# Performance work log

Hardware: AMD Instinct MI355X
Metric: run time of the kernel (lower is better)

Reference implementation:

```python
import jax, jax.numpy as jnp
import numpy as np

K = 20
EPS = 1e-5  # BatchNorm eps
SLOPE = 0.2  # LeakyReLU negative slope


def _lrelu(y):
    return jnp.where(y > 0, y, SLOPE * y)


def _knn_idx(x):
    # x: [B, C, N] -> idx [B, N, K] of nearest neighbors (largest of negative sq dist)
    inner = -2.0 * jnp.einsum('bcn,bcm->bnm', x, x)
    xx = jnp.sum(x * x, axis=1)  # [B, N]
    pd = -xx[:, :, None] - inner - xx[:, None, :]  # [B, N, N]
    return jax.lax.top_k(pd, K)[1]


def _graph_feature(x):
    # x: [B, C, N] -> [B, 2C, N, K] = cat(neighbor - center, center)
    idx = _knn_idx(x)
    xt = jnp.transpose(x, (0, 2, 1))  # [B, N, C]
    nb = jax.vmap(lambda f, i: f[i])(xt, idx)  # [B, N, K, C]
    ctr = xt[:, :, None, :]
    feat = jnp.concatenate([nb - ctr, jnp.broadcast_to(ctr, nb.shape)], axis=-1)
    return jnp.transpose(feat, (0, 3, 1, 2))


def _bn(y, p, ch_axis):
    g, b, m, v = p[0], p[1], p[2], p[3]
    shape = [1] * y.ndim
    shape[ch_axis] = -1
    scale = (g / jnp.sqrt(v + EPS)).reshape(shape)
    return (y - m.reshape(shape)) * scale + b.reshape(shape)


def _conv_block(x, w, bn):
    f = _graph_feature(x)  # [B, 2C_in, N, K]
    y = jnp.einsum('bcnk,oc->bonk', f, w)  # 1x1 conv, no bias
    y = _lrelu(_bn(y, bn, 1))
    return jnp.max(y, axis=-1)  # max over K neighbors -> [B, C_out, N]


def setup_inputs() -> dict:
    key = jax.random.key(0)
    ks = jax.random.split(key, 20)
    B, N = 8, 1024
    inp = {
        'x': jax.random.normal(ks[0], (B, 3, N), jnp.float32),
        'w0': jax.random.normal(ks[1], (64, 6), jnp.float32) * 0.1,
        'w1': jax.random.normal(ks[2], (64, 128), jnp.float32) * 0.1,
        'w2': jax.random.normal(ks[3], (128, 128), jnp.float32) * 0.1,
        'w3': jax.random.normal(ks[4], (256, 256), jnp.float32) * 0.1,
        'bn0': jax.random.uniform(ks[5], (4, 64), jnp.float32) + 0.1,
        'bn1': jax.random.uniform(ks[6], (4, 64), jnp.float32) + 0.1,
        'bn2': jax.random.uniform(ks[7], (4, 128), jnp.float32) + 0.1,
        'bn3': jax.random.uniform(ks[8], (4, 256), jnp.float32) + 0.1,
        'we': jax.random.normal(ks[9], (1024, 512), jnp.float32) * 0.05,
        'bne': jax.random.uniform(ks[10], (4, 1024), jnp.float32) + 0.1,
        'wf0': jax.random.normal(ks[11], (512, 2048), jnp.float32) * 0.02,
        'bnf0': jax.random.uniform(ks[12], (4, 512), jnp.float32) + 0.1,
        'wf1': jax.random.normal(ks[13], (256, 512), jnp.float32) * 0.05,
        'bnf1': jax.random.uniform(ks[14], (4, 256), jnp.float32) + 0.1,
        'wfin': jax.random.normal(ks[15], (64, 256), jnp.float32) * 0.05,
        'bfin': jax.random.normal(ks[16], (64,), jnp.float32) * 0.05,
    }
    return inp


def reference(x, w0, w1, w2, w3, bn0, bn1, bn2, bn3, we, bne, wf0, bnf0, wf1, bnf1, wfin, bfin):
    B = x.shape[0]
    x1 = _conv_block(x, w0, bn0)   # [B, 64, N]
    x2 = _conv_block(x1, w1, bn1)  # [B, 64, N]
    x3 = _conv_block(x2, w2, bn2)  # [B, 128, N]
    x4 = _conv_block(x3, w3, bn3)  # [B, 256, N]
    cat = jnp.concatenate([x1, x2, x3, x4], axis=1)  # [B, 512, N]
    e = _lrelu(_bn(jnp.einsum('bcn,oc->bon', cat, we), bne, 1))  # [B, 1024, N]
    p1 = jnp.max(e, axis=-1)
    p2 = jnp.mean(e, axis=-1)
    h = jnp.concatenate([p1, p2], axis=1)  # [B, 2048]
    h = _lrelu(_bn(h @ wf0.T, bnf0, 1))  # [B, 512]; dropout is eval-mode identity
    h = _lrelu(_bn(h @ wf1.T, bnf1, 1))  # [B, 256]
    return h @ wfin.T + bfin  # [B, 64]
```

## Files before the change

kernel.cpp:

```cpp
#include <hip/hip_runtime.h>
#include <math.h>

#define N_PTS 1024
#define BATCH 8
#define KNN 20
#define EPSB 1e-5f
#define SLOPE 0.2f

typedef __attribute__((ext_vector_type(8))) short short8;
typedef __attribute__((ext_vector_type(4))) float f32x4;
typedef unsigned short ushort_t;
typedef unsigned long long u64;

__device__ __forceinline__ float lrelu(float y) { return y > 0.f ? y : SLOPE * y; }

__device__ __forceinline__ ushort_t f2bf(float f) {
    union { float f; unsigned u; } v; v.f = f;
    unsigned r = v.u + 0x7FFF + ((v.u >> 16) & 1);
    return (ushort_t)(r >> 16);
}

__device__ __forceinline__ void wprep_one(const float* __restrict__ w, float* __restrict__ wpt,
                                          int C, int Cout, int g) {
    int M2 = 2 * Cout;
    if (g >= C * M2) return;
    int c = g / M2, m = g - c * M2;
    float v;
    if (m < Cout) v = w[(size_t)m * 2 * C + c];
    else { int o = m - Cout; v = w[(size_t)o * 2 * C + C + c] - w[(size_t)o * 2 * C + c]; }
    wpt[(size_t)c * M2 + m] = v;
}

__global__ void prep_kernel(const float* __restrict__ we, ushort_t* __restrict__ weh,
                            const float* __restrict__ w0, float* __restrict__ wpt0,
                            const float* __restrict__ w1, float* __restrict__ wpt1,
                            const float* __restrict__ w2, float* __restrict__ wpt2,
                            const float* __restrict__ w3, float* __restrict__ wpt3) {
    int bx = blockIdx.x, tid = threadIdx.x;
    if (bx < 512) {
        int g = bx * 256 + tid;
        float4 v = ((const float4*)we)[g];
        ushort4 o;
        o.x = f2bf(v.x); o.y = f2bf(v.y); o.z = f2bf(v.z); o.w = f2bf(v.w);
        ((ushort4*)weh)[g] = o;
    } else if (bx < 514) {
        wprep_one(w0, wpt0, 3, 64, (bx - 512) * 256 + tid);
    } else if (bx < 546) {
        wprep_one(w1, wpt1, 64, 64, (bx - 514) * 256 + tid);
    } else if (bx < 610) {
        wprep_one(w2, wpt2, 64, 128, (bx - 546) * 256 + tid);
    } else {
        wprep_one(w3, wpt3, 128, 256, (bx - 610) * 256 + tid);
    }
}

__global__ void __launch_bounds__(64)
xx_kernel(const float* __restrict__ x, float* __restrict__ xx, int C, int bstride) {
    int b = blockIdx.y;
    int n = blockIdx.x * 64 + threadIdx.x;
    const float* xb = x + (size_t)b * bstride + n;
    float s = 0.f;
    #pragma unroll 4
    for (int c = 0; c < C; c++) { float v = xb[(size_t)c * N_PTS]; s += v * v; }
    xx[b * N_PTS + n] = s;
}

__global__ void __launch_bounds__(256)
pdabv_kernel(const float* __restrict__ x, const float* __restrict__ wpt,
             const float* __restrict__ xx,
             float* __restrict__ pd, float* __restrict__ A, float* __restrict__ Bv,
             int C, int Cout, int bstride, int pdTiles) {
    int b = blockIdx.z;
    int nt = blockIdx.y;
    int bx = blockIdx.x;
    int tid = threadIdx.x;
    int tx = tid & 15, ty = tid >> 4;
    int n0 = nt * 128;
    __shared__ float sU1[16][128];
    const float* xb = x + (size_t)b * bstride;
    float acc[8][8] = {};

    bool isPd = bx < pdTiles;
    int m0 = isPd ? bx * 128 : (bx - pdTiles) * 128;
    const float* Abase = isPd ? (xb + n0) : (wpt + m0);
    int Astride = isPd ? N_PTS : 2 * Cout;
    const float* Bbase = isPd ? (xb + m0) : (xb + n0);

    int fr = tid >> 5, fcol = (tid & 31) * 4;
    for (int c0 = 0; c0 < C; c0 += 16) {
        int kmax = C - c0; if (kmax > 16) kmax = 16;
        {
            float4 z = {0.f, 0.f, 0.f, 0.f};
            int ca = c0 + fr, cb2 = c0 + fr + 8;
            float4 v0 = (ca < C) ? *(const float4*)&Bbase[(size_t)ca * N_PTS + fcol] : z;
            float4 v1 = (cb2 < C) ? *(const float4*)&Bbase[(size_t)cb2 * N_PTS + fcol] : z;
            *(float4*)&sU1[fr][fcol] = v0;
            *(float4*)&sU1[fr + 8][fcol] = v1;
        }
        __syncthreads();
        if (kmax == 16) {
            #pragma unroll 4
            for (int k = 0; k < 16; k++) {
                const float* ap = Abase + (size_t)(c0 + k) * Astride;
                float4 a0 = *(const float4*)&ap[ty * 4];
                float4 a1 = *(const float4*)&ap[64 + ty * 4];
                float4 b0 = *(const float4*)&sU1[k][tx * 4];
                float4 b1 = *(const float4*)&sU1[k][64 + tx * 4];
                float av[8] = {a0.x, a0.y, a0.z, a0.w, a1.x, a1.y, a1.z, a1.w};
                float bw[8] = {b0.x, b0.y, b0.z, b0.w, b1.x, b1.y, b1.z, b1.w};
                #pragma unroll
                for (int i = 0; i < 8; i++)
                    #pragma unroll
                    for (int j = 0; j < 8; j++) acc[i][j] += av[i] * bw[j];
            }
        } else {
            for (int k = 0; k < kmax; k++) {
                const float* ap = Abase + (size_t)(c0 + k) * Astride;
                float4 a0 = *(const float4*)&ap[ty * 4];
                float4 a1 = *(const float4*)&ap[64 + ty * 4];
                float4 b0 = *(const float4*)&sU1[k][tx * 4];
                float4 b1 = *(const float4*)&sU1[k][64 + tx * 4];
                float av[8] = {a0.x, a0.y, a0.z, a0.w, a1.x, a1.y, a1.z, a1.w};
                float bw[8] = {b0.x, b0.y, b0.z, b0.w, b1.x, b1.y, b1.z, b1.w};
                #pragma unroll
                for (int i = 0; i < 8; i++)
                    #pragma unroll
                    for (int j = 0; j < 8; j++) acc[i][j] += av[i] * bw[j];
            }
        }
        __syncthreads();
    }

    if (isPd) {
        float xm[8];
        const float* xxb = xx + b * N_PTS + m0;
        *(float4*)&xm[0] = *(const float4*)&xxb[tx * 4];
        *(float4*)&xm[4] = *(const float4*)&xxb[64 + tx * 4];
        #pragma unroll
        for (int i = 0; i < 8; i++) {
            int n = n0 + (i >> 2) * 64 + ty * 4 + (i & 3);
            float* prow = pd + ((size_t)(b * N_PTS + n)) * N_PTS;
            for (int jh = 0; jh < 2; jh++) {
                float4 o;
                o.x = 2.f * acc[i][jh * 4 + 0] - xm[jh * 4 + 0];
                o.y = 2.f * acc[i][jh * 4 + 1] - xm[jh * 4 + 1];
                o.z = 2.f * acc[i][jh * 4 + 2] - xm[jh * 4 + 2];
                o.w = 2.f * acc[i][jh * 4 + 3] - xm[jh * 4 + 3];
                *(float4*)&prow[m0 + jh * 64 + tx * 4] = o;
            }
        }
    } else {
        #pragma unroll
        for (int i = 0; i < 8; i++) {
            int rowm = m0 + (i >> 2) * 64 + ty * 4 + (i & 3);
            float* dst = (rowm < Cout) ? (A + ((size_t)b * Cout + rowm) * N_PTS)
                                       : (Bv + ((size_t)b * Cout + rowm - Cout) * N_PTS);
            for (int jh = 0; jh < 2; jh++) {
                float4 o;
                o.x = acc[i][jh * 4 + 0];
                o.y = acc[i][jh * 4 + 1];
                o.z = acc[i][jh * 4 + 2];
                o.w = acc[i][jh * 4 + 3];
                *(float4*)&dst[n0 + jh * 64 + tx * 4] = o;
            }
        }
    }
}

__global__ void __launch_bounds__(256)
topk_kernel(const float* __restrict__ pd, int* __restrict__ idx) {
    int wid = threadIdx.x >> 6;
    int row = blockIdx.x * 4 + wid;
    int lane = threadIdx.x & 63;
    __shared__ u64 Sk[4][64];
    const float* p = pd + (size_t)row * N_PTS;
    float v[16];
    for (int q = 0; q < 4; q++) {
        float4 t = *(const float4*)&p[lane * 16 + q * 4];
        v[q * 4 + 0] = t.x; v[q * 4 + 1] = t.y; v[q * 4 + 2] = t.z; v[q * 4 + 3] = t.w;
    }
    float lmax = v[0];
    #pragma unroll
    for (int j = 1; j < 16; j++) lmax = fmaxf(lmax, v[j]);
    float s = lmax;
    #pragma unroll
    for (int k = 2; k <= 64; k <<= 1) {
        #pragma unroll
        for (int j = k >> 1; j > 0; j >>= 1) {
            float o = __shfl_xor(s, j, 64);
            bool takeMin = (((lane & k) == 0) == ((lane & j) == 0));
            float mn = fminf(s, o), mx = fmaxf(s, o);
            s = takeMin ? mn : mx;
        }
    }
    float tp = __shfl(s, 44, 64);
    unsigned hm = 0;
    #pragma unroll
    for (int j = 0; j < 16; j++) hm |= (v[j] >= tp ? 1u : 0u) << j;
    int cnt = __popc(hm);
    int incl = cnt;
    #pragma unroll
    for (int d = 1; d < 64; d <<= 1) {
        int o = __shfl_up(incl, d, 64);
        if (lane >= d) incl += o;
    }
    int total = __shfl(incl, 63, 64);
    int pos = incl - cnt;
    if (total <= 64) {
        #pragma unroll
        for (int j = 0; j < 16; j++) {
            if (hm & (1u << j)) {
                unsigned u = __float_as_uint(v[j]);
                unsigned msk = ((unsigned)((int)u >> 31)) | 0x80000000u;
                Sk[wid][pos] = ((u64)(u ^ msk) << 32) | (unsigned)(1023 - (lane * 16 + j));
                pos++;
            }
        }
        u64 key = (lane < total) ? Sk[wid][lane] : 0ull;
        #pragma unroll
        for (int k = 2; k <= 64; k <<= 1) {
            #pragma unroll
            for (int j = k >> 1; j > 0; j >>= 1) {
                u64 o = __shfl_xor(key, j, 64);
                bool takeMin = (((lane & k) == 0) == ((lane & j) == 0));
                bool sgt = key > o;
                key = (sgt != takeMin) ? key : o;
            }
        }
        if (lane >= 44) {
            int m = 1023 - (int)(unsigned)(key & 0xFFFFFFFFu);
            idx[row * KNN + (63 - lane)] = m;
        }
    } else {
        for (int kk = 0; kk < KNN; kk++) {
            float bv = v[0]; int bj = 0;
            #pragma unroll
            for (int j = 1; j < 16; j++) if (v[j] > bv) { bv = v[j]; bj = j; }
            int bi = lane * 16 + bj;
            for (int d = 32; d > 0; d >>= 1) {
                float ov = __shfl_down(bv, d, 64);
                int oi = __shfl_down(bi, d, 64);
                if (ov > bv || (ov == bv && oi < bi)) { bv = ov; bi = oi; }
            }
            bi = __shfl(bi, 0, 64);
            if ((bi >> 4) == lane) {
                #pragma unroll
                for (int j = 0; j < 16; j++) if (j == (bi & 15)) v[j] = -INFINITY;
            }
            if (lane == 0) idx[row * KNN + kk] = bi;
        }
    }
}

__global__ void __launch_bounds__(256)
topk0_kernel(const float* __restrict__ x, int* __restrict__ idx) {
    int wid = threadIdx.x >> 6;
    int row = blockIdx.x * 4 + wid;
    int lane = threadIdx.x & 63;
    __shared__ u64 Sk[4][64];
    int b = row >> 10, n = row & 1023;
    const float* xb = x + (size_t)b * 3 * N_PTS;
    float xr0 = xb[n], xr1 = xb[N_PTS + n], xr2 = xb[2 * N_PTS + n];
    float v[16];
    for (int q = 0; q < 4; q++) {
        int base = lane * 16 + q * 4;
        float4 c0 = *(const float4*)&xb[base];
        float4 c1 = *(const float4*)&xb[N_PTS + base];
        float4 c2 = *(const float4*)&xb[2 * N_PTS + base];
        float a0[4] = {c0.x, c0.y, c0.z, c0.w};
        float a1[4] = {c1.x, c1.y, c1.z, c1.w};
        float a2[4] = {c2.x, c2.y, c2.z, c2.w};
        #pragma unroll
        for (int j = 0; j < 4; j++) {
            float d = 0.f;
            d += xr0 * a0[j]; d += xr1 * a1[j]; d += xr2 * a2[j];
            float sq = 0.f;
            sq += a0[j] * a0[j]; sq += a1[j] * a1[j]; sq += a2[j] * a2[j];
            v[q * 4 + j] = 2.f * d - sq;
        }
    }
    float lmax = v[0];
    #pragma unroll
    for (int j = 1; j < 16; j++) lmax = fmaxf(lmax, v[j]);
    float s = lmax;
    #pragma unroll
    for (int k = 2; k <= 64; k <<= 1) {
        #pragma unroll
        for (int j = k >> 1; j > 0; j >>= 1) {
            float o = __shfl_xor(s, j, 64);
            bool takeMin = (((lane & k) == 0) == ((lane & j) == 0));
            float mn = fminf(s, o), mx = fmaxf(s, o);
            s = takeMin ? mn : mx;
        }
    }
    float tp = __shfl(s, 44, 64);
    unsigned hm = 0;
    #pragma unroll
    for (int j = 0; j < 16; j++) hm |= (v[j] >= tp ? 1u : 0u) << j;
    int cnt = __popc(hm);
    int incl = cnt;
    #pragma unroll
    for (int d = 1; d < 64; d <<= 1) {
        int o = __shfl_up(incl, d, 64);
        if (lane >= d) incl += o;
    }
    int total = __shfl(incl, 63, 64);
    int pos = incl - cnt;
    if (total <= 64) {
        #pragma unroll
        for (int j = 0; j < 16; j++) {
            if (hm & (1u << j)) {
                unsigned u = __float_as_uint(v[j]);
                unsigned msk = ((unsigned)((int)u >> 31)) | 0x80000000u;
                Sk[wid][pos] = ((u64)(u ^ msk) << 32) | (unsigned)(1023 - (lane * 16 + j));
                pos++;
            }
        }
        u64 key = (lane < total) ? Sk[wid][lane] : 0ull;
        #pragma unroll
        for (int k = 2; k <= 64; k <<= 1) {
            #pragma unroll
            for (int j = k >> 1; j > 0; j >>= 1) {
                u64 o = __shfl_xor(key, j, 64);
                bool takeMin = (((lane & k) == 0) == ((lane & j) == 0));
                bool sgt = key > o;
                key = (sgt != takeMin) ? key : o;
            }
        }
        if (lane >= 44) {
            int m = 1023 - (int)(unsigned)(key & 0xFFFFFFFFu);
            idx[row * KNN + (63 - lane)] = m;
        }
    } else {
        for (int kk = 0; kk < KNN; kk++) {
            float bv = v[0]; int bj = 0;
            #pragma unroll
            for (int j = 1; j < 16; j++) if (v[j] > bv) { bv = v[j]; bj = j; }
            int bi = lane * 16 + bj;
            for (int d = 32; d > 0; d >>= 1) {
                float ov = __shfl_down(bv, d, 64);
                int oi = __shfl_down(bi, d, 64);
                if (ov > bv || (ov == bv && oi < bi)) { bv = ov; bi = oi; }
            }
            bi = __shfl(bi, 0, 64);
            if ((bi >> 4) == lane) {
                #pragma unroll
                for (int j = 0; j < 16; j++) if (j == (bi & 15)) v[j] = -INFINITY;
            }
            if (lane == 0) idx[row * KNN + kk] = bi;
        }
    }
}

__global__ void __launch_bounds__(256)
gmax_kernel(const float* __restrict__ A, const float* __restrict__ Bv,
            const int* __restrict__ idx, const float* __restrict__ bnp,
            float* __restrict__ out, int Cout, int outStrideB) {
    int b = blockIdx.z;
    int n0 = blockIdx.x * 64;
    int o0 = blockIdx.y * 4;
    int tid = threadIdx.x;
    __shared__ int sidx[64 * 21];
    __shared__ float sA[4][N_PTS];
    for (int t = tid; t < 64 * KNN; t += 256) {
        int nl = t / KNN, k = t - nl * KNN;
        sidx[nl * 21 + k] = idx[(b * N_PTS + n0) * KNN + t];
    }
    const float* Abase = A + ((size_t)b * Cout + o0) * N_PTS;
    for (int q = 0; q < 4; q++) {
        int f = q * 256 + tid;
        int r = f >> 8, c4 = (f & 255) * 4;
        *(float4*)&sA[r][c4] = *(const float4*)&Abase[(size_t)r * N_PTS + c4];
    }
    __syncthreads();
    int nl = tid & 63, ol = tid >> 6;
    float best = -INFINITY;
    #pragma unroll
    for (int k = 0; k < KNN; k++) {
        int j = sidx[nl * 21 + k];
        best = fmaxf(best, sA[ol][j]);
    }
    int o = o0 + ol;
    int n = n0 + nl;
    float pre = best + Bv[((size_t)b * Cout + o) * N_PTS + n];
    float g = bnp[o], bb = bnp[Cout + o], m = bnp[2 * Cout + o], vv = bnp[3 * Cout + o];
    float scale = g / sqrtf(vv + EPSB);
    out[(size_t)b * outStrideB + (size_t)o * N_PTS + n] = lrelu((pre - m) * scale + bb);
}

__global__ void catT_kernel(const float* __restrict__ cat, ushort_t* __restrict__ catT) {
    int b = blockIdx.z, ct = blockIdx.y, nt = blockIdx.x;
    int tid = threadIdx.x;
    __shared__ float tile[64][65];
    const float* cb = cat + (size_t)b * 512 * N_PTS;
    for (int q = 0; q < 16; q++) {
        int e = q * 256 + tid;
        int c = e >> 6, n = e & 63;
        tile[c][n] = cb[(size_t)(ct * 64 + c) * N_PTS + nt * 64 + n];
    }
    __syncthreads();
    for (int q = 0; q < 16; q++) {
        int e = q * 256 + tid;
        int n = e >> 6, c = e & 63;
        catT[((size_t)b * N_PTS + nt * 64 + n) * 512 + ct * 64 + c] = f2bf(tile[c][n]);
    }
}

__global__ void __launch_bounds__(256)
gemm6_mfma(const ushort_t* __restrict__ weh, const ushort_t* __restrict__ catT,
           const float* __restrict__ bne,
           float* __restrict__ pmax, float* __restrict__ psum) {
    int b = blockIdx.z, ot = blockIdx.y, nt = blockIdx.x;
    int tid = threadIdx.x;
    int w = tid >> 6, lane = tid & 63, q = lane >> 4, lr = lane & 15;
    int mblk = w >> 1, nblk = w & 1;
    __shared__ __align__(16) ushort_t sA[128 * 40];
    __shared__ __align__(16) ushort_t sB[128 * 40];
    __shared__ float sa[128], sc[128];
    __shared__ float redmax[128][2], redsum[128][2];
    int o0 = ot * 128, n0 = nt * 128;
    if (tid < 128) {
        int o = o0 + tid;
        float g = bne[o], bb = bne[1024 + o], m = bne[2048 + o], vv = bne[3072 + o];
        float scale = g / sqrtf(vv + EPSB);
        sa[tid] = scale; sc[tid] = bb - m * scale;
    }
    f32x4 acc[4][4] = {};
    const ushort_t* cT = catT + (size_t)b * N_PTS * 512;
    int r0 = tid >> 2, s = tid & 3;
    for (int k0 = 0; k0 < 512; k0 += 32) {
        __syncthreads();
        for (int h = 0; h < 2; h++) {
            int r = r0 + h * 64;
            *(short8*)&sA[r * 40 + s * 8] = *(const short8*)(weh + (size_t)(o0 + r) * 512 + k0 + s * 8);
            *(short8*)&sB[r * 40 + s * 8] = *(const short8*)(cT  + (size_t)(n0 + r) * 512 + k0 + s * 8);
        }
        __syncthreads();
        short8 af[4], bfr[4];
        for (int mi = 0; mi < 4; mi++)
            af[mi] = *(const short8*)&sA[(mblk * 64 + mi * 16 + lr) * 40 + q * 8];
        for (int ni = 0; ni < 4; ni++)
            bfr[ni] = *(const short8*)&sB[(nblk * 64 + ni * 16 + lr) * 40 + q * 8];
        for (int mi = 0; mi < 4; mi++)
            for (int ni = 0; ni < 4; ni++)
                acc[mi][ni] = __builtin_amdgcn_mfma_f32_16x16x32_bf16(af[mi], bfr[ni], acc[mi][ni], 0, 0, 0);
    }
    for (int mi = 0; mi < 4; mi++) {
        for (int r = 0; r < 4; r++) {
            int row = mblk * 64 + mi * 16 + q * 4 + r;
            float a = sa[row], c = sc[row];
            float mx = -INFINITY, sm = 0.f;
            for (int ni = 0; ni < 4; ni++) {
                float y = lrelu(acc[mi][ni][r] * a + c);
                mx = fmaxf(mx, y); sm += y;
            }
            for (int msk = 1; msk < 16; msk <<= 1) {
                mx = fmaxf(mx, __shfl_xor(mx, msk, 16));
                sm += __shfl_xor(sm, msk, 16);
            }
            if (lr == 0) { redmax[row][nblk] = mx; redsum[row][nblk] = sm; }
        }
    }
    __syncthreads();
    if (tid < 128) {
        float mx = fmaxf(redmax[tid][0], redmax[tid][1]);
        float sm = redsum[tid][0] + redsum[tid][1];
        int o = o0 + tid;
        pmax[((size_t)(b * 1024 + o)) * 8 + nt] = mx;
        psum[((size_t)(b * 1024 + o)) * 8 + nt] = sm;
    }
}

__global__ void pool_reduce_kernel(const float* __restrict__ pmax, const float* __restrict__ psum,
                                   float* __restrict__ h0) {
    int g = blockIdx.x * 256 + threadIdx.x;
    int b = g >> 10, o = g & 1023;
    float mx = -INFINITY, sm = 0.f;
    for (int t = 0; t < 8; t++) { mx = fmaxf(mx, pmax[g * 8 + t]); sm += psum[g * 8 + t]; }
    h0[(size_t)b * 2048 + o] = mx;
    h0[(size_t)b * 2048 + 1024 + o] = sm * (1.0f / 1024.0f);
}

__global__ void fc_kernel(const float* __restrict__ in, const float* __restrict__ w,
                          const float* __restrict__ bnp, const float* __restrict__ bias,
                          float* __restrict__ out, int Cin, int Cout, int mode) {
    int blk = blockIdx.x;
    int b = blk / Cout, o = blk % Cout;
    int lane = threadIdx.x;
    const float* inb = in + (size_t)b * Cin;
    const float* wo = w + (size_t)o * Cin;
    float acc = 0.f;
    for (int c = lane; c < Cin; c += 64) acc += inb[c] * wo[c];
    for (int s = 32; s > 0; s >>= 1) acc += __shfl_down(acc, s, 64);
    if (lane == 0) {
        float y = acc;
        if (mode == 0) {
            float g = bnp[o], bb = bnp[Cout + o], m = bnp[2 * Cout + o], vv = bnp[3 * Cout + o];
            y = lrelu((y - m) * (g / sqrtf(vv + EPSB)) + bb);
        } else {
            y += bias[o];
        }
        out[(size_t)b * Cout + o] = y;
    }
}

extern "C" void kernel_launch(void* const* d_in, const int* in_sizes, int n_in,
                              void* d_out, int out_size, void* d_ws, size_t ws_size,
                              hipStream_t stream) {
    const float* x    = (const float*)d_in[0];
    const float* w0   = (const float*)d_in[1];
    const float* w1   = (const float*)d_in[2];
    const float* w2   = (const float*)d_in[3];
    const float* w3   = (const float*)d_in[4];
    const float* bn0  = (const float*)d_in[5];
    const float* bn1  = (const float*)d_in[6];
    const float* bn2  = (const float*)d_in[7];
    const float* bn3  = (const float*)d_in[8];
    const float* we   = (const float*)d_in[9];
    const float* bne  = (const float*)d_in[10];
    const float* wf0  = (const float*)d_in[11];
    const float* bnf0 = (const float*)d_in[12];
    const float* wf1  = (const float*)d_in[13];
    const float* bnf1 = (const float*)d_in[14];
    const float* wfin = (const float*)d_in[15];
    const float* bfin = (const float*)d_in[16];

    float* ws = (float*)d_ws;
    size_t off = 0;
    float* cat  = ws + off; off += (size_t)BATCH * 512 * N_PTS;
    float* pd   = ws + off; off += (size_t)BATCH * N_PTS * N_PTS;
    float* A    = ws + off; off += (size_t)BATCH * 256 * N_PTS;
    float* Bv   = ws + off; off += (size_t)BATCH * 256 * N_PTS;
    float* xxv  = ws + off; off += (size_t)BATCH * N_PTS;
    float* pmax = ws + off; off += (size_t)BATCH * N_PTS * 8;
    float* psum = ws + off; off += (size_t)BATCH * N_PTS * 8;
    float* h0   = ws + off; off += (size_t)BATCH * 2048;
    float* h1   = ws + off; off += (size_t)BATCH * 512;
    float* h2   = ws + off; off += (size_t)BATCH * 256;
    int*   idx  = (int*)(ws + off); off += (size_t)BATCH * N_PTS * KNN;
    ushort_t* weh  = (ushort_t*)(ws + off); off += (size_t)(1024 * 512) / 2;
    ushort_t* catT = (ushort_t*)(ws + off); off += (size_t)BATCH * N_PTS * 512 / 2;
    float* wpt0 = ws + off; off += 3 * 128;
    float* wpt1 = ws + off; off += 64 * 128;
    float* wpt2 = ws + off; off += 64 * 256;
    float* wpt3 = ws + off; off += 128 * 512;

    const int CSTR = 512 * N_PTS;
    const int topkBlocks = BATCH * N_PTS / 4;

    prep_kernel<<<866, 256, 0, stream>>>(we, weh, w0, wpt0, w1, wpt1, w2, wpt2, w3, wpt3);

    pdabv_kernel<<<dim3(1, 8, BATCH), 256, 0, stream>>>(x, wpt0, xxv, pd, A, Bv, 3, 64, 3 * N_PTS, 0);
    topk0_kernel<<<topkBlocks, 256, 0, stream>>>(x, idx);
    gmax_kernel<<<dim3(16, 16, BATCH), 256, 0, stream>>>(A, Bv, idx, bn0, cat, 64, CSTR);

    xx_kernel<<<dim3(16, BATCH), 64, 0, stream>>>(cat, xxv, 64, CSTR);
    pdabv_kernel<<<dim3(9, 8, BATCH), 256, 0, stream>>>(cat, wpt1, xxv, pd, A, Bv, 64, 64, CSTR, 8);
    topk_kernel<<<topkBlocks, 256, 0, stream>>>(pd, idx);
    gmax_kernel<<<dim3(16, 16, BATCH), 256, 0, stream>>>(A, Bv, idx, bn1, cat + 64 * N_PTS, 64, CSTR);

    xx_kernel<<<dim3(16, BATCH), 64, 0, stream>>>(cat + 64 * N_PTS, xxv, 64, CSTR);
    pdabv_kernel<<<dim3(10, 8, BATCH), 256, 0, stream>>>(cat + 64 * N_PTS, wpt2, xxv, pd, A, Bv, 64, 128, CSTR, 8);
    topk_kernel<<<topkBlocks, 256, 0, stream>>>(pd, idx);
    gmax_kernel<<<dim3(16, 32, BATCH), 256, 0, stream>>>(A, Bv, idx, bn2, cat + 128 * N_PTS, 128, CSTR);

    xx_kernel<<<dim3(16, BATCH), 64, 0, stream>>>(cat + 128 * N_PTS, xxv, 128, CSTR);
    pdabv_kernel<<<dim3(12, 8, BATCH), 256, 0, stream>>>(cat + 128 * N_PTS, wpt3, xxv, pd, A, Bv, 128, 256, CSTR, 8);
    topk_kernel<<<topkBlocks, 256, 0, stream>>>(pd, idx);
    gmax_kernel<<<dim3(16, 64, BATCH), 256, 0, stream>>>(A, Bv, idx, bn3, cat + 256 * N_PTS, 256, CSTR);

    catT_kernel<<<dim3(16, 8, BATCH), 256, 0, stream>>>(cat, catT);
    gemm6_mfma<<<dim3(8, 8, BATCH), 256, 0, stream>>>(weh, catT, bne, pmax, psum);
    pool_reduce_kernel<<<32, 256, 0, stream>>>(pmax, psum, h0);

    fc_kernel<<<BATCH * 512, 64, 0, stream>>>(h0, wf0, bnf0, nullptr, h1, 2048, 512, 0);
    fc_kernel<<<BATCH * 256, 64, 0, stream>>>(h1, wf1, bnf1, nullptr, h2, 512, 256, 0);
    fc_kernel<<<BATCH * 64, 64, 0, stream>>>(h2, wfin, nullptr, bfin, (float*)d_out, 256, 64, 1);
}
```

Measured before the change: 360.0 us.

## Double-buffer both GEMM operands in shared memory and fuse squared-norm computation

The pairwise-distance/feature GEMM kernel now stages both the A and B tiles in double-buffered shared memory, prefetching the next K-chunk into registers while computing the current one. Previously A was read directly from global memory. The per-point squared norms are accumulated inside the pd GEMM from the staged B values, which removes the separate xx_kernel launches and their buffer. The cost is double the shared memory per block, which may lower occupancy.

```diff
diff --git a/kernel.cpp b/kernel.cpp
--- a/kernel.cpp
+++ b/kernel.cpp
@@ -54,20 +54,8 @@
     }
 }
 
-__global__ void __launch_bounds__(64)
-xx_kernel(const float* __restrict__ x, float* __restrict__ xx, int C, int bstride) {
-    int b = blockIdx.y;
-    int n = blockIdx.x * 64 + threadIdx.x;
-    const float* xb = x + (size_t)b * bstride + n;
-    float s = 0.f;
-    #pragma unroll 4
-    for (int c = 0; c < C; c++) { float v = xb[(size_t)c * N_PTS]; s += v * v; }
-    xx[b * N_PTS + n] = s;
-}
-
 __global__ void __launch_bounds__(256)
 pdabv_kernel(const float* __restrict__ x, const float* __restrict__ wpt,
-             const float* __restrict__ xx,
              float* __restrict__ pd, float* __restrict__ A, float* __restrict__ Bv,
              int C, int Cout, int bstride, int pdTiles) {
     int b = blockIdx.z;
@@ -76,66 +64,61 @@
     int tid = threadIdx.x;
     int tx = tid & 15, ty = tid >> 4;
     int n0 = nt * 128;
-    __shared__ float sU1[16][128];
+    __shared__ float sA[2][16][128];
+    __shared__ float sB[2][16][128];
     const float* xb = x + (size_t)b * bstride;
+    int fr = tid >> 5, fcol = (tid & 31) * 4;
     float acc[8][8] = {};
 
-    bool isPd = bx < pdTiles;
-    int m0 = isPd ? bx * 128 : (bx - pdTiles) * 128;
-    const float* Abase = isPd ? (xb + n0) : (wpt + m0);
-    int Astride = isPd ? N_PTS : 2 * Cout;
-    const float* Bbase = isPd ? (xb + m0) : (xb + n0);
-
-    int fr = tid >> 5, fcol = (tid & 31) * 4;
-    for (int c0 = 0; c0 < C; c0 += 16) {
-        int kmax = C - c0; if (kmax > 16) kmax = 16;
-        {
-            float4 z = {0.f, 0.f, 0.f, 0.f};
-            int ca = c0 + fr, cb2 = c0 + fr + 8;
-            float4 v0 = (ca < C) ? *(const float4*)&Bbase[(size_t)ca * N_PTS + fcol] : z;
-            float4 v1 = (cb2 < C) ? *(const float4*)&Bbase[(size_t)cb2 * N_PTS + fcol] : z;
-            *(float4*)&sU1[fr][fcol] = v0;
-            *(float4*)&sU1[fr + 8][fcol] = v1;
-        }
+    if (bx < pdTiles) {
+        int m0 = bx * 128;
+        const float* An = xb + n0;
+        const float* Bm = xb + m0;
+        float xm[8] = {};
+        float4 a0r, a1r, b0r, b1r;
+        a0r = *(const float4*)&An[(size_t)fr * N_PTS + fcol];
+        a1r = *(const float4*)&An[(size_t)(fr + 8) * N_PTS + fcol];
+        b0r = *(const float4*)&Bm[(size_t)fr * N_PTS + fcol];
+        b1r = *(const float4*)&Bm[(size_t)(fr + 8) * N_PTS + fcol];
+        *(float4*)&sA[0][fr][fcol] = a0r;
+        *(float4*)&sA[0][fr + 8][fcol] = a1r;
+        *(float4*)&sB[0][fr][fcol] = b0r;
+        *(float4*)&sB[0][fr + 8][fcol] = b1r;
         __syncthreads();
-        if (kmax == 16) {
-            #pragma unroll 4
+        int nc = C >> 4;
+        for (int cc = 0; cc < nc; cc++) {
+            int cur = cc & 1;
+            if (cc + 1 < nc) {
+                int c0 = (cc + 1) * 16;
+                a0r = *(const float4*)&An[(size_t)(c0 + fr) * N_PTS + fcol];
+                a1r = *(const float4*)&An[(size_t)(c0 + fr + 8) * N_PTS + fcol];
+                b0r = *(const float4*)&Bm[(size_t)(c0 + fr) * N_PTS + fcol];
+                b1r = *(const float4*)&Bm[(size_t)(c0 + fr + 8) * N_PTS + fcol];
+            }
+            #pragma unroll
             for (int k = 0; k < 16; k++) {
-                const float* ap = Abase + (size_t)(c0 + k) * Astride;
-                float4 a0 = *(const float4*)&ap[ty * 4];
-                float4 a1 = *(const float4*)&ap[64 + ty * 4];
-                float4 b0 = *(const float4*)&sU1[k][tx * 4];
-                float4 b1 = *(const float4*)&sU1[k][64 + tx * 4];
+                float4 a0 = *(const float4*)&sA[cur][k][ty * 4];
+                float4 a1 = *(const float4*)&sA[cur][k][64 + ty * 4];
+                float4 b0 = *(const float4*)&sB[cur][k][tx * 4];
+                float4 b1 = *(const float4*)&sB[cur][k][64 + tx * 4];
                 float av[8] = {a0.x, a0.y, a0.z, a0.w, a1.x, a1.y, a1.z, a1.w};
                 float bw[8] = {b0.x, b0.y, b0.z, b0.w, b1.x, b1.y, b1.z, b1.w};
                 #pragma unroll
                 for (int i = 0; i < 8; i++)
                     #pragma unroll
                     for (int j = 0; j < 8; j++) acc[i][j] += av[i] * bw[j];
-            }
-        } else {
-            for (int k = 0; k < kmax; k++) {
-                const float* ap = Abase + (size_t)(c0 + k) * Astride;
-                float4 a0 = *(const float4*)&ap[ty * 4];
-                float4 a1 = *(const float4*)&ap[64 + ty * 4];
-                float4 b0 = *(const float4*)&sU1[k][tx * 4];
-                float4 b1 = *(const float4*)&sU1[k][64 + tx * 4];
-                float av[8] = {a0.x, a0.y, a0.z, a0.w, a1.x, a1.y, a1.z, a1.w};
-                float bw[8] = {b0.x, b0.y, b0.z, b0.w, b1.x, b1.y, b1.z, b1.w};
                 #pragma unroll
-                for (int i = 0; i < 8; i++)
-                    #pragma unroll
-                    for (int j = 0; j < 8; j++) acc[i][j] += av[i] * bw[j];
-            }
-        }
-        __syncthreads();
-    }
-
-    if (isPd) {
-        float xm[8];
-        const float* xxb = xx + b * N_PTS + m0;
-        *(float4*)&xm[0] = *(const float4*)&xxb[tx * 4];
-        *(float4*)&xm[4] = *(const float4*)&xxb[64 + tx * 4];
+                for (int j = 0; j < 8; j++) xm[j] += bw[j] * bw[j];
+            }
+            if (cc + 1 < nc) {
+                int nb = cur ^ 1;
+                *(float4*)&sA[nb][fr][fcol] = a0r;
+                *(float4*)&sA[nb][fr + 8][fcol] = a1r;
+                *(float4*)&sB[nb][fr][fcol] = b0r;
+                *(float4*)&sB[nb][fr + 8][fcol] = b1r;
+                __syncthreads();
+            }
+        }
         #pragma unroll
         for (int i = 0; i < 8; i++) {
             int n = n0 + (i >> 2) * 64 + ty * 4 + (i & 3);
@@ -150,6 +133,73 @@
             }
         }
     } else {
+        int m0 = (bx - pdTiles) * 128;
+        int M2 = 2 * Cout;
+        const float* Wm = wpt + m0;
+        const float* Xn = xb + n0;
+        float4 a0r, a1r, b0r, b1r;
+        float4 z = {0.f, 0.f, 0.f, 0.f};
+        {
+            int ca = fr, cb2 = fr + 8;
+            a0r = (ca < C) ? *(const float4*)&Wm[(size_t)ca * M2 + fcol] : z;
+            a1r = (cb2 < C) ? *(const float4*)&Wm[(size_t)cb2 * M2 + fcol] : z;
+            b0r = (ca < C) ? *(const float4*)&Xn[(size_t)ca * N_PTS + fcol] : z;
+            b1r = (cb2 < C) ? *(const float4*)&Xn[(size_t)cb2 * N_PTS + fcol] : z;
+        }
+        *(float4*)&sA[0][fr][fcol] = a0r;
+        *(float4*)&sA[0][fr + 8][fcol] = a1r;
+        *(float4*)&sB[0][fr][fcol] = b0r;
+        *(float4*)&sB[0][fr + 8][fcol] = b1r;
+        __syncthreads();
+        int nc = (C + 15) >> 4;
+        for (int cc = 0; cc < nc; cc++) {
+            int cur = cc & 1;
+            if (cc + 1 < nc) {
+                int c0 = (cc + 1) * 16;
+                int ca = c0 + fr, cb2 = c0 + fr + 8;
+                a0r = (ca < C) ? *(const float4*)&Wm[(size_t)ca * M2 + fcol] : z;
+                a1r = (cb2 < C) ? *(const float4*)&Wm[(size_t)cb2 * M2 + fcol] : z;
+                b0r = (ca < C) ? *(const float4*)&Xn[(size_t)ca * N_PTS + fcol] : z;
+                b1r = (cb2 < C) ? *(const float4*)&Xn[(size_t)cb2 * N_PTS + fcol] : z;
+            }
+            int kmax = C - cc * 16; if (kmax > 16) kmax = 16;
+            if (kmax == 16) {
+                #pragma unroll
+                for (int k = 0; k < 16; k++) {
+                    float4 a0 = *(const float4*)&sA[cur][k][ty * 4];
+                    float4 a1 = *(const float4*)&sA[cur][k][64 + ty * 4];
+                    float4 b0 = *(const float4*)&sB[cur][k][tx * 4];
+                    float4 b1 = *(const float4*)&sB[cur][k][64 + tx * 4];
+                    float av[8] = {a0.x, a0.y, a0.z, a0.w, a1.x, a1.y, a1.z, a1.w};
+                    float bw[8] = {b0.x, b0.y, b0.z, b0.w, b1.x, b1.y, b1.z, b1.w};
+                    #pragma unroll
+                    for (int i = 0; i < 8; i++)
+                        #pragma unroll
+                        for (int j = 0; j < 8; j++) acc[i][j] += av[i] * bw[j];
+                }
+            } else {
+                for (int k = 0; k < kmax; k++) {
+                    float4 a0 = *(const float4*)&sA[cur][k][ty * 4];
+                    float4 a1 = *(const float4*)&sA[cur][k][64 + ty * 4];
+                    float4 b0 = *(const float4*)&sB[cur][k][tx * 4];
+                    float4 b1 = *(const float4*)&sB[cur][k][64 + tx * 4];
+                    float av[8] = {a0.x, a0.y, a0.z, a0.w, a1.x, a1.y, a1.z, a1.w};
+                    float bw[8] = {b0.x, b0.y, b0.z, b0.w, b1.x, b1.y, b1.z, b1.w};
+                    #pragma unroll
+                    for (int i = 0; i < 8; i++)
+                        #pragma unroll
+                        for (int j = 0; j < 8; j++) acc[i][j] += av[i] * bw[j];
+                }
+            }
+            if (cc + 1 < nc) {
+                int nb = cur ^ 1;
+                *(float4*)&sA[nb][fr][fcol] = a0r;
+                *(float4*)&sA[nb][fr + 8][fcol] = a1r;
+                *(float4*)&sB[nb][fr][fcol] = b0r;
+                *(float4*)&sB[nb][fr + 8][fcol] = b1r;
+                __syncthreads();
+            }
+        }
         #pragma unroll
         for (int i = 0; i < 8; i++) {
             int rowm = m0 + (i >> 2) * 64 + ty * 4 + (i & 3);
@@ -531,7 +581,6 @@
     float* pd   = ws + off; off += (size_t)BATCH * N_PTS * N_PTS;
     float* A    = ws + off; off += (size_t)BATCH * 256 * N_PTS;
     float* Bv   = ws + off; off += (size_t)BATCH * 256 * N_PTS;
-    float* xxv  = ws + off; off += (size_t)BATCH * N_PTS;
     float* pmax = ws + off; off += (size_t)BATCH * N_PTS * 8;
     float* psum = ws + off; off += (size_t)BATCH * N_PTS * 8;
     float* h0   = ws + off; off += (size_t)BATCH * 2048;
@@ -550,22 +599,19 @@
 
     prep_kernel<<<866, 256, 0, stream>>>(we, weh, w0, wpt0, w1, wpt1, w2, wpt2, w3, wpt3);
 
-    pdabv_kernel<<<dim3(1, 8, BATCH), 256, 0, stream>>>(x, wpt0, xxv, pd, A, Bv, 3, 64, 3 * N_PTS, 0);
+    pdabv_kernel<<<dim3(1, 8, BATCH), 256, 0, stream>>>(x, wpt0, pd, A, Bv, 3, 64, 3 * N_PTS, 0);
     topk0_kernel<<<topkBlocks, 256, 0, stream>>>(x, idx);
     gmax_kernel<<<dim3(16, 16, BATCH), 256, 0, stream>>>(A, Bv, idx, bn0, cat, 64, CSTR);
 
-    xx_kernel<<<dim3(16, BATCH), 64, 0, stream>>>(cat, xxv, 64, CSTR);
-    pdabv_kernel<<<dim3(9, 8, BATCH), 256, 0, stream>>>(cat, wpt1, xxv, pd, A, Bv, 64, 64, CSTR, 8);
+    pdabv_kernel<<<dim3(9, 8, BATCH), 256, 0, stream>>>(cat, wpt1, pd, A, Bv, 64, 64, CSTR, 8);
     topk_kernel<<<topkBlocks, 256, 0, stream>>>(pd, idx);
     gmax_kernel<<<dim3(16, 16, BATCH), 256, 0, stream>>>(A, Bv, idx, bn1, cat + 64 * N_PTS, 64, CSTR);
 
-    xx_kernel<<<dim3(16, BATCH), 64, 0, stream>>>(cat + 64 * N_PTS, xxv, 64, CSTR);
-    pdabv_kernel<<<dim3(10, 8, BATCH), 256, 0, stream>>>(cat + 64 * N_PTS, wpt2, xxv, pd, A, Bv, 64, 128, CSTR, 8);
+    pdabv_kernel<<<dim3(10, 8, BATCH), 256, 0, stream>>>(cat + 64 * N_PTS, wpt2, pd, A, Bv, 64, 128, CSTR, 8);
     topk_kernel<<<topkBlocks, 256, 0, stream>>>(pd, idx);
     gmax_kernel<<<dim3(16, 32, BATCH), 256, 0, stream>>>(A, Bv, idx, bn2, cat + 128 * N_PTS, 128, CSTR);
 
-    xx_kernel<<<dim3(16, BATCH), 64, 0, stream>>>(cat + 128 * N_PTS, xxv, 128, CSTR);
-    pdabv_kernel<<<dim3(12, 8, BATCH), 256, 0, stream>>>(cat + 128 * N_PTS, wpt3, xxv, pd, A, Bv, 128, 256, CSTR, 8);
+    pdabv_kernel<<<dim3(12, 8, BATCH), 256, 0, stream>>>(cat + 128 * N_PTS, wpt3, pd, A, Bv, 128, 256, CSTR, 8);
     topk_kernel<<<topkBlocks, 256, 0, stream>>>(pd, idx);
     gmax_kernel<<<dim3(16, 64, BATCH), 256, 0, stream>>>(A, Bv, idx, bn3, cat + 256 * N_PTS, 256, CSTR);
 
```

Result: slower. 368.1 us (+2.3%).
